# Kernel tuning notes

Hardware: AMD Instinct MI355X
Metric: run time of the kernel (lower is better)

## Reference

```python
import jax, jax.numpy as jnp
import numpy as np

D = 256        # embedding_dim
K = 4096       # num_embeddings
DECAY = 0.99
EPS = 1e-05
COMMIT = 0.25


def setup_inputs() -> dict:
    key = jax.random.key(0)
    kx, ke = jax.random.split(key)
    x = jax.random.normal(kx, (32, 1024, D), dtype=jnp.float32)
    # variance_scaling(scale=1.0, mode='fan_in', distribution='uniform') on (D, K): fan_in = D
    limit = np.sqrt(3.0 / D).astype(np.float32)
    embeddings = jax.random.uniform(ke, (D, K), dtype=jnp.float32, minval=-limit, maxval=limit)
    return {
        'x': x,
        'embeddings': embeddings,
        'ema_counter': jnp.zeros((), jnp.float32),
        'ema_hidden_cluster': jnp.zeros((K,), jnp.float32),
        'ema_hidden_dw': jnp.zeros((D, K), jnp.float32),
    }


def reference(x, embeddings, ema_counter, ema_hidden_cluster, ema_hidden_dw):
    flat = x.reshape(-1, D)  # [N, D]
    # squared euclidean distance to each code: [N, K]
    distance = (jnp.sum(flat ** 2, axis=1, keepdims=True)
                - 2.0 * jnp.matmul(flat, embeddings)
                + jnp.sum(embeddings ** 2, axis=0, keepdims=True))
    encoding_indices = jnp.argmax(-distance, axis=1)           # [N]
    encodings = jax.nn.one_hot(encoding_indices, K, dtype=distance.dtype)  # [N, K]
    idx = encoding_indices.reshape(x.shape[:-1])               # [B, T]
    quantized = jnp.take(embeddings.T, idx, axis=0)            # [B, T, D]

    e_latent_loss = jnp.mean((quantized - x) ** 2)
    q_latent_loss = jnp.mean((quantized - x) ** 2)
    vq_loss = q_latent_loss + COMMIT * e_latent_loss

    # EMA codebook update (training=True path); debiased EMA per the module
    counter = ema_counter + 1.0
    bias = 1.0 - jnp.power(DECAY, counter)
    cluster_hidden = ema_hidden_cluster * DECAY + jnp.sum(encodings, axis=0) * (1.0 - DECAY)
    cluster_avg = cluster_hidden / bias                         # [K]
    dw = jnp.matmul(flat.T, encodings)                          # [D, K]
    dw_hidden = ema_hidden_dw * DECAY + dw * (1.0 - DECAY)
    dw_avg = dw_hidden / bias                                   # [D, K]
    n = jnp.sum(cluster_avg)
    cluster_norm = (cluster_avg + EPS) / (n + K * EPS) * n
    new_embeddings = dw_avg / cluster_norm[None, :]             # [D, K]

    avg_probs = jnp.mean(encodings, axis=0)
    perplexity = jnp.exp(-jnp.sum(avg_probs * jnp.log(avg_probs + 1e-10)))
    return quantized, vq_loss, perplexity, idx, new_embeddings
```

## Files before the change

### kernel.cpp

```cpp
#include <hip/hip_runtime.h>
#include <math.h>

#define N_TOK 32768
#define DIM   256
#define KCODE 4096

#define WS_E2      0
#define WS_COUNTS  4096
#define WS_LOSSP   8192
#define WS_SCAL    8448
#define WS_CNORM   8512
#define WS_IDX     12608
#define WS_EHS     307520
#define WS_DWT     1356096
#define WS_CARRYV  2404672
#define WS_CARRYI  2437440
#define WS_OFFS    2470208
#define WS_WOFF    2474304

#define OUT_Q      0
#define OUT_LOSS   8388608
#define OUT_PERP   8388609
#define OUT_IDX    8388610
#define OUT_EMB    8421378

#define EH_PLANE   1048576

typedef _Float16 f16x8 __attribute__((ext_vector_type(8)));
typedef _Float16 f16x4 __attribute__((ext_vector_type(4)));
typedef float    f32x4 __attribute__((ext_vector_type(4)));

__global__ void k_split_e(const float* __restrict__ emb, unsigned short* __restrict__ ehs_,
                          float* __restrict__ e2)
{
    __shared__ float tile[32][33];
    _Float16* ehs = (_Float16*)ehs_;
    int t  = threadIdx.x;
    int tx = t & 31, iy = t >> 5;
    int k0 = blockIdx.x * 32, d0 = blockIdx.y * 32;
#pragma unroll
    for (int j = 0; j < 4; ++j)
        tile[iy + 8 * j][tx] = emb[(size_t)(d0 + iy + 8 * j) * KCODE + k0 + tx];
    __syncthreads();
    int code = k0 + tx;
    size_t base = (size_t)(((code >> 8) * 8) + (d0 >> 5)) * 8192 + (code & 255) * 32 + iy * 4;
    f16x4 h1, h2;
    float ssq = 0.0f;
#pragma unroll
    for (int j = 0; j < 4; ++j) {
        float v = tile[iy * 4 + j][tx];
        ssq += v * v;
        _Float16 a = (_Float16)v;
        h1[j] = a;
        h2[j] = (_Float16)(v - (float)a);
    }
    *(f16x4*)(ehs + base)            = h1;
    *(f16x4*)(ehs + EH_PLANE + base) = h2;
    atomicAdd(&e2[code], ssq);
}

__global__ __launch_bounds__(256, 2)
void k_argmin(const float* __restrict__ x, const unsigned short* __restrict__ ehs_,
              const float* __restrict__ e2, int* __restrict__ idx_out,
              float* __restrict__ carryV, int* __restrict__ carryI,
              float* __restrict__ out_idxf, float* __restrict__ counts,
              int ct0, int phase)
{
    __shared__ __align__(16) _Float16 Ah[2][64][256];

    const _Float16* ehs = (const _Float16*)ehs_;

    const int t    = threadIdx.x;
    const int lane = t & 63, w = t >> 6;
    const int lo   = lane & 15, q = lane >> 4;
    const int row0 = blockIdx.x * 64;

    {
        int m = t >> 3, kb = (t & 7) * 32;
#pragma unroll
        for (int rr = 0; rr < 2; ++rr) {
            int mm = m + 32 * rr;
            const float* src = x + (size_t)(row0 + mm) * DIM + kb;
#pragma unroll
            for (int g = 0; g < 4; ++g) {
                f32x4 f0 = __builtin_nontemporal_load((const f32x4*)(src + g * 8));
                f32x4 f1 = __builtin_nontemporal_load((const f32x4*)(src + g * 8 + 4));
                f16x8 h1, h2;
#pragma unroll
                for (int j = 0; j < 4; ++j) {
                    _Float16 a = (_Float16)f0[j];
                    h1[j] = a; h2[j] = (_Float16)(f0[j] - (float)a);
                    _Float16 b = (_Float16)f1[j];
                    h1[j + 4] = b; h2[j + 4] = (_Float16)(f1[j] - (float)b);
                }
                int grp = ((kb >> 3) + g) ^ (mm & 7);
                *(f16x8*)&Ah[0][mm][grp * 8] = h1;
                *(f16x8*)&Ah[1][mm][grp * 8] = h2;
            }
        }
    }
    __syncthreads();

    float best[16];
    int   bidx[16];
#pragma unroll
    for (int s = 0; s < 16; ++s) { best[s] = 3.4e38f; bidx[s] = 0; }

    const _Float16* ehp1 = ehs + (size_t)(w * 64 + lo) * 32 + q * 8;
    const _Float16* ehp2 = ehp1 + EH_PLANE;

    f16x8 b1f[2][4], b2f[2][4];

    {
        const size_t so0 = (size_t)(ct0 * 8) * 8192;
#pragma unroll
        for (int nf = 0; nf < 4; ++nf) {
            b1f[0][nf] = *(const f16x8*)(ehp1 + so0 + nf * 512);
            b2f[0][nf] = *(const f16x8*)(ehp2 + so0 + nf * 512);
        }
    }

    for (int ct = ct0; ct < ct0 + 8; ++ct) {
        float e2r[4];
#pragma unroll
        for (int nf = 0; nf < 4; ++nf)
            e2r[nf] = e2[ct * 256 + w * 64 + nf * 16 + lo];

        f32x4 acc[4][4];
#pragma unroll
        for (int mf = 0; mf < 4; ++mf)
#pragma unroll
            for (int nf = 0; nf < 4; ++nf) acc[mf][nf] = (f32x4)0.0f;

#pragma unroll
        for (int ks = 0; ks < 8; ++ks) {
            const int cur = ks & 1, nxt = cur ^ 1;
            const int so  = ct * 8 + ks;

            if (ks < 7 || ct < ct0 + 7) {
                const size_t po = (size_t)(so + 1) * 8192;
#pragma unroll
                for (int nf = 0; nf < 4; ++nf) {
                    b1f[nxt][nf] = *(const f16x8*)(ehp1 + po + nf * 512);
                    b2f[nxt][nf] = *(const f16x8*)(ehp2 + po + nf * 512);
                }
            }
            __builtin_amdgcn_sched_barrier(0);

            const int agrp = ((ks * 4 + q) ^ (lo & 7)) * 8;
            f16x8 a1[4], a2[4];
#pragma unroll
            for (int mf = 0; mf < 4; ++mf)
                a2[mf] = *(const f16x8*)&Ah[1][mf * 16 + lo][agrp];
#pragma unroll
            for (int mf = 0; mf < 4; ++mf)
                a1[mf] = *(const f16x8*)&Ah[0][mf * 16 + lo][agrp];

#pragma unroll
            for (int nf = 0; nf < 4; ++nf) {
#pragma unroll
                for (int mf = 0; mf < 4; ++mf)
                    acc[mf][nf] = __builtin_amdgcn_mfma_f32_16x16x32_f16(a2[mf], b1f[cur][nf], acc[mf][nf], 0, 0, 0);
#pragma unroll
                for (int mf = 0; mf < 4; ++mf)
                    acc[mf][nf] = __builtin_amdgcn_mfma_f32_16x16x32_f16(a1[mf], b2f[cur][nf], acc[mf][nf], 0, 0, 0);
#pragma unroll
                for (int mf = 0; mf < 4; ++mf)
                    acc[mf][nf] = __builtin_amdgcn_mfma_f32_16x16x32_f16(a1[mf], b1f[cur][nf], acc[mf][nf], 0, 0, 0);
            }
        }

#pragma unroll
        for (int nf = 0; nf < 4; ++nf) {
            int cl = w * 64 + nf * 16 + lo;
            float e2v = e2r[nf];
#pragma unroll
            for (int mf = 0; mf < 4; ++mf)
#pragma unroll
                for (int r = 0; r < 4; ++r) {
                    float dist = fmaf(-2.0f, acc[mf][nf][r], e2v);
                    int s = mf * 4 + r;
                    if (dist < best[s]) { best[s] = dist; bidx[s] = ct * 256 + cl; }
                }
        }
    }

    __syncthreads();
    float* rv = (float*)&Ah[0][0][0];
    int*   ri = (int*)(((char*)&Ah[0][0][0]) + 16384);
#pragma unroll
    for (int s = 0; s < 16; ++s) {
        int row = (s >> 2) * 16 + q * 4 + (s & 3);
        rv[row * 64 + w * 16 + lo] = best[s];
        ri[row * 64 + w * 16 + lo] = bidx[s];
    }
    __syncthreads();
    if (t < 64) {
        float bv; int bi;
        if (phase) { bv = carryV[row0 + t]; bi = carryI[row0 + t]; }
        else       { bv = 3.4e38f; bi = 0x40000000; }
        for (int jj = 0; jj < 64; ++jj) {
            int j = (jj + t) & 63;
            float v = rv[t * 64 + j];
            int  ii = ri[t * 64 + j];
            if (v < bv || (v == bv && ii < bi)) { bv = v; bi = ii; }
        }
        if (phase) {
            idx_out[row0 + t] = bi;
            out_idxf[row0 + t] = (float)bi;
            atomicAdd(&counts[bi], 1.0f);
        } else {
            carryV[row0 + t] = bv; carryI[row0 + t] = bi;
        }
    }
}

__global__ void k_scan(const float* __restrict__ counts, int* __restrict__ offs,
                       int* __restrict__ woff)
{
    __shared__ int ps[256];
    int t = threadIdx.x;
    int local[16];
    int s = 0;
#pragma unroll
    for (int j = 0; j < 16; ++j) {
        local[j] = s;
        s += (int)counts[t * 16 + j];
    }
    ps[t] = s;
    __syncthreads();
    for (int off = 1; off < 256; off <<= 1) {
        int v = (t >= off) ? ps[t - off] : 0;
        __syncthreads();
        ps[t] += v;
        __syncthreads();
    }
    int base = (t > 0) ? ps[t - 1] : 0;
#pragma unroll
    for (int j = 0; j < 16; ++j) {
        int o = base + local[j];
        offs[t * 16 + j] = o;
        woff[t * 16 + j] = o;
    }
}

__global__ void k_scatter(const int* __restrict__ idx, int* __restrict__ woff,
                          int* __restrict__ rowlist)
{
    int n = blockIdx.x * 256 + threadIdx.x;
    int k = idx[n];
    int pos = atomicAdd(&woff[k], 1);
    rowlist[pos] = n;
}

__global__ void k_dw(const float* __restrict__ x, const unsigned short* __restrict__ ehs_,
                     const int* __restrict__ rowlist, const int* __restrict__ offs,
                     const float* __restrict__ counts, float* __restrict__ dwT,
                     float* __restrict__ out_q, float* __restrict__ lossp)
{
    __shared__ __align__(16) float es[256];
    __shared__ __align__(16) float red[4][256];
    const _Float16* ehs = (const _Float16*)ehs_;
    int k = blockIdx.x, t = threadIdx.x;
    int lane = t & 63, w = t >> 6;
    size_t base = (size_t)(((k >> 8) * 8) + (t >> 5)) * 8192 + (k & 255) * 32 + (t & 31);
    float e = (float)ehs[base] + (float)ehs[EH_PLANE + base];
    es[t] = e;
    int start = offs[k];
    int cnt   = (int)counts[k];
    __syncthreads();
    float4 ev = *(const float4*)&es[lane * 4];
    float4 acc = {0.0f, 0.0f, 0.0f, 0.0f};
    float sq = 0.0f;
    for (int j = w; j < cnt; j += 4) {
        int n = rowlist[start + j];
        float4 xv = *(const float4*)&x[(size_t)n * DIM + lane * 4];
        acc.x += xv.x; acc.y += xv.y; acc.z += xv.z; acc.w += xv.w;
        sq += xv.x * xv.x + xv.y * xv.y + xv.z * xv.z + xv.w * xv.w;
        *(float4*)&out_q[(size_t)n * DIM + lane * 4] = ev;
    }
    *(float4*)&red[w][lane * 4] = acc;
    __syncthreads();
    float s = red[0][t] + red[1][t] + red[2][t] + red[3][t];
    dwT[(size_t)k * DIM + t] = s;
    float v1 = es[t] * s;
    float v2 = e * e;
    float v3 = sq;
#pragma unroll
    for (int off = 32; off > 0; off >>= 1) {
        v1 += __shfl_down(v1, off, 64);
        v2 += __shfl_down(v2, off, 64);
        v3 += __shfl_down(v3, off, 64);
    }
    __syncthreads();
    if (lane == 0) { red[0][w] = v1; red[1][w] = v2; red[2][w] = v3; }
    __syncthreads();
    if (t == 0 && cnt > 0) {
        float dot = red[0][0] + red[0][1] + red[0][2] + red[0][3];
        float e2t = red[1][0] + red[1][1] + red[1][2] + red[1][3];
        float sqt = red[2][0] + red[2][1] + red[2][2] + red[2][3];
        atomicAdd(&lossp[k & 255], (float)cnt * e2t - 2.0f * dot + sqt);
    }
}

__global__ void k_finalize(const float* __restrict__ counts, const float* __restrict__ lossp,
                           const float* __restrict__ ema_counter,
                           const float* __restrict__ ema_cluster,
                           float* __restrict__ cnorm, float* __restrict__ scal,
                           float* __restrict__ out)
{
    __shared__ float red[256];
    int t = threadIdx.x;
    float ls = lossp[t];
    float ent = 0.0f, casum = 0.0f;
    float ca[16];
#pragma unroll
    for (int j = 0; j < 16; ++j) {
        int k = j * 256 + t;
        float c = counts[k];
        float p = c * (1.0f / 32768.0f);
        ent += p * logf(p + 1e-10f);
        ca[j] = ema_cluster[k] * 0.99f + c * 0.01f;
        casum += ca[j];
    }
    red[t] = ls; __syncthreads();
    for (int o = 128; o > 0; o >>= 1) { if (t < o) red[t] += red[t + o]; __syncthreads(); }
    float loss_tot = red[0]; __syncthreads();
    red[t] = ent; __syncthreads();
    for (int o = 128; o > 0; o >>= 1) { if (t < o) red[t] += red[t + o]; __syncthreads(); }
    float ent_tot = red[0]; __syncthreads();
    red[t] = casum; __syncthreads();
    for (int o = 128; o > 0; o >>= 1) { if (t < o) red[t] += red[t + o]; __syncthreads(); }
    float casum_tot = red[0]; __syncthreads();

    float bias = 1.0f - powf(0.99f, ema_counter[0] + 1.0f);
    float n = casum_tot / bias;
    float inv = n / (n + 4096.0f * 1e-5f);
#pragma unroll
    for (int j = 0; j < 16; ++j) {
        int k = j * 256 + t;
        cnorm[k] = (ca[j] / bias + 1e-5f) * inv;
    }
    if (t == 0) {
        out[OUT_LOSS] = 1.25f * loss_tot * (1.0f / (32768.0f * 256.0f));
        out[OUT_PERP] = expf(-ent_tot);
        scal[0] = bias;
    }
}

__global__ void k_newemb(const float* __restrict__ dwT, const float* __restrict__ ema_dw,
                         const float* __restrict__ cnorm, const float* __restrict__ scal,
                         float* __restrict__ out_emb)
{
    __shared__ float tile[32][33];
    int t = threadIdx.x;
    int tx = t & 31, iy = t >> 5;
    int k0 = blockIdx.x * 32, d0 = blockIdx.y * 32;
#pragma unroll
    for (int j = 0; j < 4; ++j)
        tile[iy + 8 * j][tx] = dwT[(size_t)(k0 + iy + 8 * j) * DIM + d0 + tx];
    __syncthreads();
    float inv_bias = 1.0f / scal[0];
    float cn = cnorm[k0 + tx];
#pragma unroll
    for (int j = 0; j < 4; ++j) {
        int d = d0 + iy + 8 * j;
        float dwv = tile[tx][iy + 8 * j];
        float hid = ema_dw[(size_t)d * KCODE + k0 + tx] * 0.99f + dwv * 0.01f;
        out_emb[(size_t)d * KCODE + k0 + tx] = hid * inv_bias / cn;
    }
}

extern "C" void kernel_launch(void* const* d_in, const int* in_sizes, int n_in,
                              void* d_out, int out_size, void* d_ws, size_t ws_size,
                              hipStream_t stream)
{
    const float* x           = (const float*)d_in[0];
    const float* emb         = (const float*)d_in[1];
    const float* ema_counter = (const float*)d_in[2];
    const float* ema_cluster = (const float*)d_in[3];
    const float* ema_dw      = (const float*)d_in[4];
    float* out = (float*)d_out;
    float* ws  = (float*)d_ws;

    float* e2     = ws + WS_E2;
    float* counts = ws + WS_COUNTS;
    float* lossp  = ws + WS_LOSSP;
    float* scal   = ws + WS_SCAL;
    float* cnorm  = ws + WS_CNORM;
    int*   idxw   = (int*)(ws + WS_IDX);
    unsigned short* ehs = (unsigned short*)(ws + WS_EHS);
    float* dwT    = ws + WS_DWT;
    float* carryV = ws + WS_CARRYV;
    int*   carryI = (int*)(ws + WS_CARRYI);
    int*   rowlist= (int*)(ws + WS_CARRYV);
    int*   offs   = (int*)(ws + WS_OFFS);
    int*   woff   = (int*)(ws + WS_WOFF);

    hipMemsetAsync(e2, 0, (size_t)WS_CNORM * sizeof(float), stream);

    k_split_e<<<dim3(128, 8), 256, 0, stream>>>(emb, ehs, e2);
    k_argmin<<<512, 256, 0, stream>>>(x, ehs, e2, idxw, carryV, carryI,
                                      out + OUT_IDX, counts, 0, 0);
    k_argmin<<<512, 256, 0, stream>>>(x, ehs, e2, idxw, carryV, carryI,
                                      out + OUT_IDX, counts, 8, 1);
    k_scan<<<1, 256, 0, stream>>>(counts, offs, woff);
    k_scatter<<<128, 256, 0, stream>>>(idxw, woff, rowlist);
    k_dw<<<4096, 256, 0, stream>>>(x, ehs, rowlist, offs, counts, dwT,
                                   out + OUT_Q, lossp);
    k_finalize<<<1, 256, 0, stream>>>(counts, lossp, ema_counter, ema_cluster,
                                      cnorm, scal, out);
    k_newemb<<<dim3(128, 8), 256, 0, stream>>>(dwT, ema_dw, cnorm, scal, out + OUT_EMB);
}
```

Measured before the change: 316.2 us.

## Double argmin block to 512 threads with narrower per-wave code tiles

Raises the argmin kernel from 4 to 8 waves per block, with each wave covering 32 codes per tile instead of 64. This halves the accumulator and B-fragment registers per wave. The software double-buffered prefetch of the codebook fragments is dropped in favour of more waves hiding latency. The final reduction now scans 128 partial results per row, and the x staging loop drops from two rows per thread to one. The risks are losing the explicit prefetch overlap and a longer serial reduction.

```diff
diff --git a/kernel.cpp b/kernel.cpp
--- a/kernel.cpp
+++ b/kernel.cpp
@@ -59,7 +59,7 @@
     atomicAdd(&e2[code], ssq);
 }
 
-__global__ __launch_bounds__(256, 2)
+__global__ __launch_bounds__(512, 2)
 void k_argmin(const float* __restrict__ x, const unsigned short* __restrict__ ehs_,
               const float* __restrict__ e2, int* __restrict__ idx_out,
               float* __restrict__ carryV, int* __restrict__ carryI,
@@ -77,26 +77,22 @@
 
     {
         int m = t >> 3, kb = (t & 7) * 32;
-#pragma unroll
-        for (int rr = 0; rr < 2; ++rr) {
-            int mm = m + 32 * rr;
-            const float* src = x + (size_t)(row0 + mm) * DIM + kb;
-#pragma unroll
-            for (int g = 0; g < 4; ++g) {
-                f32x4 f0 = __builtin_nontemporal_load((const f32x4*)(src + g * 8));
-                f32x4 f1 = __builtin_nontemporal_load((const f32x4*)(src + g * 8 + 4));
-                f16x8 h1, h2;
-#pragma unroll
-                for (int j = 0; j < 4; ++j) {
-                    _Float16 a = (_Float16)f0[j];
-                    h1[j] = a; h2[j] = (_Float16)(f0[j] - (float)a);
-                    _Float16 b = (_Float16)f1[j];
-                    h1[j + 4] = b; h2[j + 4] = (_Float16)(f1[j] - (float)b);
-                }
-                int grp = ((kb >> 3) + g) ^ (mm & 7);
-                *(f16x8*)&Ah[0][mm][grp * 8] = h1;
-                *(f16x8*)&Ah[1][mm][grp * 8] = h2;
+        const float* src = x + (size_t)(row0 + m) * DIM + kb;
+#pragma unroll
+        for (int g = 0; g < 4; ++g) {
+            f32x4 f0 = __builtin_nontemporal_load((const f32x4*)(src + g * 8));
+            f32x4 f1 = __builtin_nontemporal_load((const f32x4*)(src + g * 8 + 4));
+            f16x8 h1, h2;
+#pragma unroll
+            for (int j = 0; j < 4; ++j) {
+                _Float16 a = (_Float16)f0[j];
+                h1[j] = a; h2[j] = (_Float16)(f0[j] - (float)a);
+                _Float16 b = (_Float16)f1[j];
+                h1[j + 4] = b; h2[j + 4] = (_Float16)(f1[j] - (float)b);
             }
+            int grp = ((kb >> 3) + g) ^ (m & 7);
+            *(f16x8*)&Ah[0][m][grp * 8] = h1;
+            *(f16x8*)&Ah[1][m][grp * 8] = h2;
         }
     }
     __syncthreads();
@@ -106,73 +102,57 @@
 #pragma unroll
     for (int s = 0; s < 16; ++s) { best[s] = 3.4e38f; bidx[s] = 0; }
 
-    const _Float16* ehp1 = ehs + (size_t)(w * 64 + lo) * 32 + q * 8;
+    const _Float16* ehp1 = ehs + (size_t)(w * 32 + lo) * 32 + q * 8;
     const _Float16* ehp2 = ehp1 + EH_PLANE;
 
-    f16x8 b1f[2][4], b2f[2][4];
-
-    {
-        const size_t so0 = (size_t)(ct0 * 8) * 8192;
-#pragma unroll
-        for (int nf = 0; nf < 4; ++nf) {
-            b1f[0][nf] = *(const f16x8*)(ehp1 + so0 + nf * 512);
-            b2f[0][nf] = *(const f16x8*)(ehp2 + so0 + nf * 512);
-        }
-    }
-
     for (int ct = ct0; ct < ct0 + 8; ++ct) {
-        float e2r[4];
-#pragma unroll
-        for (int nf = 0; nf < 4; ++nf)
-            e2r[nf] = e2[ct * 256 + w * 64 + nf * 16 + lo];
-
-        f32x4 acc[4][4];
+        float e2r[2];
+#pragma unroll
+        for (int nf = 0; nf < 2; ++nf)
+            e2r[nf] = e2[ct * 256 + w * 32 + nf * 16 + lo];
+
+        f32x4 acc[4][2];
 #pragma unroll
         for (int mf = 0; mf < 4; ++mf)
 #pragma unroll
-            for (int nf = 0; nf < 4; ++nf) acc[mf][nf] = (f32x4)0.0f;
+            for (int nf = 0; nf < 2; ++nf) acc[mf][nf] = (f32x4)0.0f;
 
 #pragma unroll
         for (int ks = 0; ks < 8; ++ks) {
-            const int cur = ks & 1, nxt = cur ^ 1;
-            const int so  = ct * 8 + ks;
-
-            if (ks < 7 || ct < ct0 + 7) {
-                const size_t po = (size_t)(so + 1) * 8192;
-#pragma unroll
-                for (int nf = 0; nf < 4; ++nf) {
-                    b1f[nxt][nf] = *(const f16x8*)(ehp1 + po + nf * 512);
-                    b2f[nxt][nf] = *(const f16x8*)(ehp2 + po + nf * 512);
-                }
+            const size_t so = (size_t)(ct * 8 + ks) * 8192;
+
+            f16x8 b1[2], b2[2];
+#pragma unroll
+            for (int nf = 0; nf < 2; ++nf) {
+                b1[nf] = *(const f16x8*)(ehp1 + so + nf * 512);
+                b2[nf] = *(const f16x8*)(ehp2 + so + nf * 512);
             }
-            __builtin_amdgcn_sched_barrier(0);
 
             const int agrp = ((ks * 4 + q) ^ (lo & 7)) * 8;
             f16x8 a1[4], a2[4];
 #pragma unroll
-            for (int mf = 0; mf < 4; ++mf)
+            for (int mf = 0; mf < 4; ++mf) {
                 a2[mf] = *(const f16x8*)&Ah[1][mf * 16 + lo][agrp];
-#pragma unroll
-            for (int mf = 0; mf < 4; ++mf)
                 a1[mf] = *(const f16x8*)&Ah[0][mf * 16 + lo][agrp];
-
-#pragma unroll
-            for (int nf = 0; nf < 4; ++nf) {
+            }
+
+#pragma unroll
+            for (int nf = 0; nf < 2; ++nf) {
 #pragma unroll
                 for (int mf = 0; mf < 4; ++mf)
-                    acc[mf][nf] = __builtin_amdgcn_mfma_f32_16x16x32_f16(a2[mf], b1f[cur][nf], acc[mf][nf], 0, 0, 0);
+                    acc[mf][nf] = __builtin_amdgcn_mfma_f32_16x16x32_f16(a2[mf], b1[nf], acc[mf][nf], 0, 0, 0);
 #pragma unroll
                 for (int mf = 0; mf < 4; ++mf)
-                    acc[mf][nf] = __builtin_amdgcn_mfma_f32_16x16x32_f16(a1[mf], b2f[cur][nf], acc[mf][nf], 0, 0, 0);
+                    acc[mf][nf] = __builtin_amdgcn_mfma_f32_16x16x32_f16(a1[mf], b2[nf], acc[mf][nf], 0, 0, 0);
 #pragma unroll
                 for (int mf = 0; mf < 4; ++mf)
-                    acc[mf][nf] = __builtin_amdgcn_mfma_f32_16x16x32_f16(a1[mf], b1f[cur][nf], acc[mf][nf], 0, 0, 0);
+                    acc[mf][nf] = __builtin_amdgcn_mfma_f32_16x16x32_f16(a1[mf], b1[nf], acc[mf][nf], 0, 0, 0);
             }
         }
 
 #pragma unroll
-        for (int nf = 0; nf < 4; ++nf) {
-            int cl = w * 64 + nf * 16 + lo;
+        for (int nf = 0; nf < 2; ++nf) {
+            int cl = w * 32 + nf * 16 + lo;
             float e2v = e2r[nf];
 #pragma unroll
             for (int mf = 0; mf < 4; ++mf)
@@ -187,22 +167,22 @@
 
     __syncthreads();
     float* rv = (float*)&Ah[0][0][0];
-    int*   ri = (int*)(((char*)&Ah[0][0][0]) + 16384);
+    int*   ri = (int*)(((char*)&Ah[0][0][0]) + 32768);
 #pragma unroll
     for (int s = 0; s < 16; ++s) {
         int row = (s >> 2) * 16 + q * 4 + (s & 3);
-        rv[row * 64 + w * 16 + lo] = best[s];
-        ri[row * 64 + w * 16 + lo] = bidx[s];
+        rv[row * 128 + w * 16 + lo] = best[s];
+        ri[row * 128 + w * 16 + lo] = bidx[s];
     }
     __syncthreads();
     if (t < 64) {
         float bv; int bi;
         if (phase) { bv = carryV[row0 + t]; bi = carryI[row0 + t]; }
         else       { bv = 3.4e38f; bi = 0x40000000; }
-        for (int jj = 0; jj < 64; ++jj) {
-            int j = (jj + t) & 63;
-            float v = rv[t * 64 + j];
-            int  ii = ri[t * 64 + j];
+        for (int jj = 0; jj < 128; ++jj) {
+            int j = (jj + t * 2) & 127;
+            float v = rv[t * 128 + j];
+            int  ii = ri[t * 128 + j];
             if (v < bv || (v == bv && ii < bi)) { bv = v; bi = ii; }
         }
         if (phase) {
@@ -400,9 +380,9 @@
     hipMemsetAsync(e2, 0, (size_t)WS_CNORM * sizeof(float), stream);
 
     k_split_e<<<dim3(128, 8), 256, 0, stream>>>(emb, ehs, e2);
-    k_argmin<<<512, 256, 0, stream>>>(x, ehs, e2, idxw, carryV, carryI,
+    k_argmin<<<512, 512, 0, stream>>>(x, ehs, e2, idxw, carryV, carryI,
                                       out + OUT_IDX, counts, 0, 0);
-    k_argmin<<<512, 256, 0, stream>>>(x, ehs, e2, idxw, carryV, carryI,
+    k_argmin<<<512, 512, 0, stream>>>(x, ehs, e2, idxw, carryV, carryI,
                                       out + OUT_IDX, counts, 8, 1);
     k_scan<<<1, 256, 0, stream>>>(counts, offs, woff);
     k_scatter<<<128, 256, 0, stream>>>(idxw, woff, rowlist);
```

After: 605.7 us. 1.92x slower.

## Fuse quantized output and loss into argmin; merge scan with finalize

Applied to the files above, without the earlier changes.

The second argmin pass now computes the per-row squared norm of x while staging it, derives each row's loss as best distance plus that norm, and writes the quantized rows directly from the split-fp16 codebook. The scan and finalize kernels are merged into a single one-block kernel. k_dw is reduced to the dw accumulation only. This removes the scattered out_q writes and the per-code loss work from k_dw and saves one launch, at the cost of a longer argmin epilogue and a loss computed from the fp16-split distance. The tie-break on equal distances is also made to prefer the lower index.

```diff
diff --git a/kernel.cpp b/kernel.cpp
--- a/kernel.cpp
+++ b/kernel.cpp
@@ -64,9 +64,12 @@
               const float* __restrict__ e2, int* __restrict__ idx_out,
               float* __restrict__ carryV, int* __restrict__ carryI,
               float* __restrict__ out_idxf, float* __restrict__ counts,
+              float* __restrict__ lossp, float* __restrict__ out_q,
               int ct0, int phase)
 {
     __shared__ __align__(16) _Float16 Ah[2][64][256];
+    __shared__ float xsqp[64][8];
+    __shared__ int   bis[64];
 
     const _Float16* ehs = (const _Float16*)ehs_;
 
@@ -77,10 +80,12 @@
 
     {
         int m = t >> 3, kb = (t & 7) * 32;
+        float ssq0 = 0.0f, ssq1 = 0.0f;
 #pragma unroll
         for (int rr = 0; rr < 2; ++rr) {
             int mm = m + 32 * rr;
             const float* src = x + (size_t)(row0 + mm) * DIM + kb;
+            float ss = 0.0f;
 #pragma unroll
             for (int g = 0; g < 4; ++g) {
                 f32x4 f0 = __builtin_nontemporal_load((const f32x4*)(src + g * 8));
@@ -88,6 +93,7 @@
                 f16x8 h1, h2;
 #pragma unroll
                 for (int j = 0; j < 4; ++j) {
+                    ss += f0[j] * f0[j] + f1[j] * f1[j];
                     _Float16 a = (_Float16)f0[j];
                     h1[j] = a; h2[j] = (_Float16)(f0[j] - (float)a);
                     _Float16 b = (_Float16)f1[j];
@@ -97,14 +103,17 @@
                 *(f16x8*)&Ah[0][mm][grp * 8] = h1;
                 *(f16x8*)&Ah[1][mm][grp * 8] = h2;
             }
-        }
+            if (rr == 0) ssq0 = ss; else ssq1 = ss;
+        }
+        xsqp[m][t & 7]      = ssq0;
+        xsqp[m + 32][t & 7] = ssq1;
     }
     __syncthreads();
 
     float best[16];
     int   bidx[16];
 #pragma unroll
-    for (int s = 0; s < 16; ++s) { best[s] = 3.4e38f; bidx[s] = 0; }
+    for (int s = 0; s < 16; ++s) { best[s] = 3.4e38f; bidx[s] = 0x40000000; }
 
     const _Float16* ehp1 = ehs + (size_t)(w * 64 + lo) * 32 + q * 8;
     const _Float16* ehp2 = ehp1 + EH_PLANE;
@@ -172,7 +181,7 @@
 
 #pragma unroll
         for (int nf = 0; nf < 4; ++nf) {
-            int cl = w * 64 + nf * 16 + lo;
+            int ci = ct * 256 + w * 64 + nf * 16 + lo;
             float e2v = e2r[nf];
 #pragma unroll
             for (int mf = 0; mf < 4; ++mf)
@@ -180,7 +189,9 @@
                 for (int r = 0; r < 4; ++r) {
                     float dist = fmaf(-2.0f, acc[mf][nf][r], e2v);
                     int s = mf * 4 + r;
-                    if (dist < best[s]) { best[s] = dist; bidx[s] = ct * 256 + cl; }
+                    if (dist < best[s] || (dist == best[s] && ci < bidx[s])) {
+                        best[s] = dist; bidx[s] = ci;
+                    }
                 }
         }
     }
@@ -209,17 +220,59 @@
             idx_out[row0 + t] = bi;
             out_idxf[row0 + t] = (float)bi;
             atomicAdd(&counts[bi], 1.0f);
+            bis[t] = bi;
+            float xsq = 0.0f;
+#pragma unroll
+            for (int j = 0; j < 8; ++j) xsq += xsqp[t][j];
+            float lr = bv + xsq;
+#pragma unroll
+            for (int off = 32; off > 0; off >>= 1) lr += __shfl_down(lr, off, 64);
+            if (t == 0) atomicAdd(&lossp[blockIdx.x & 255], lr);
         } else {
             carryV[row0 + t] = bv; carryI[row0 + t] = bi;
         }
     }
-}
-
-__global__ void k_scan(const float* __restrict__ counts, int* __restrict__ offs,
-                       int* __restrict__ woff)
-{
-    __shared__ int ps[256];
+    if (phase) {
+        __syncthreads();
+        int r  = t >> 2, qs = t & 3;
+        int k  = bis[r];
+        float* dst = out_q + (size_t)(row0 + r) * DIM + qs * 64;
+        const _Float16* ehb = ehs + (size_t)((k >> 8) * 8 + qs * 2) * 8192 + (k & 255) * 32;
+#pragma unroll
+        for (int dd = 0; dd < 2; ++dd) {
+            const _Float16* p1 = ehb + dd * 8192;
+            const _Float16* p2 = p1 + EH_PLANE;
+#pragma unroll
+            for (int g = 0; g < 4; ++g) {
+                f16x8 h1 = *(const f16x8*)(p1 + g * 8);
+                f16x8 h2 = *(const f16x8*)(p2 + g * 8);
+                float4 o0, o1;
+                o0.x = (float)h1[0] + (float)h2[0];
+                o0.y = (float)h1[1] + (float)h2[1];
+                o0.z = (float)h1[2] + (float)h2[2];
+                o0.w = (float)h1[3] + (float)h2[3];
+                o1.x = (float)h1[4] + (float)h2[4];
+                o1.y = (float)h1[5] + (float)h2[5];
+                o1.z = (float)h1[6] + (float)h2[6];
+                o1.w = (float)h1[7] + (float)h2[7];
+                *(float4*)(dst + dd * 32 + g * 8)     = o0;
+                *(float4*)(dst + dd * 32 + g * 8 + 4) = o1;
+            }
+        }
+    }
+}
+
+__global__ void k_scanfin(const float* __restrict__ counts, const float* __restrict__ lossp,
+                          const float* __restrict__ ema_counter,
+                          const float* __restrict__ ema_cluster,
+                          int* __restrict__ offs, int* __restrict__ woff,
+                          float* __restrict__ cnorm, float* __restrict__ scal,
+                          float* __restrict__ out)
+{
+    __shared__ int   ps[256];
+    __shared__ float red[256];
     int t = threadIdx.x;
+
     int local[16];
     int s = 0;
 #pragma unroll
@@ -242,75 +295,7 @@
         offs[t * 16 + j] = o;
         woff[t * 16 + j] = o;
     }
-}
-
-__global__ void k_scatter(const int* __restrict__ idx, int* __restrict__ woff,
-                          int* __restrict__ rowlist)
-{
-    int n = blockIdx.x * 256 + threadIdx.x;
-    int k = idx[n];
-    int pos = atomicAdd(&woff[k], 1);
-    rowlist[pos] = n;
-}
-
-__global__ void k_dw(const float* __restrict__ x, const unsigned short* __restrict__ ehs_,
-                     const int* __restrict__ rowlist, const int* __restrict__ offs,
-                     const float* __restrict__ counts, float* __restrict__ dwT,
-                     float* __restrict__ out_q, float* __restrict__ lossp)
-{
-    __shared__ __align__(16) float es[256];
-    __shared__ __align__(16) float red[4][256];
-    const _Float16* ehs = (const _Float16*)ehs_;
-    int k = blockIdx.x, t = threadIdx.x;
-    int lane = t & 63, w = t >> 6;
-    size_t base = (size_t)(((k >> 8) * 8) + (t >> 5)) * 8192 + (k & 255) * 32 + (t & 31);
-    float e = (float)ehs[base] + (float)ehs[EH_PLANE + base];
-    es[t] = e;
-    int start = offs[k];
-    int cnt   = (int)counts[k];
-    __syncthreads();
-    float4 ev = *(const float4*)&es[lane * 4];
-    float4 acc = {0.0f, 0.0f, 0.0f, 0.0f};
-    float sq = 0.0f;
-    for (int j = w; j < cnt; j += 4) {
-        int n = rowlist[start + j];
-        float4 xv = *(const float4*)&x[(size_t)n * DIM + lane * 4];
-        acc.x += xv.x; acc.y += xv.y; acc.z += xv.z; acc.w += xv.w;
-        sq += xv.x * xv.x + xv.y * xv.y + xv.z * xv.z + xv.w * xv.w;
-        *(float4*)&out_q[(size_t)n * DIM + lane * 4] = ev;
-    }
-    *(float4*)&red[w][lane * 4] = acc;
-    __syncthreads();
-    float s = red[0][t] + red[1][t] + red[2][t] + red[3][t];
-    dwT[(size_t)k * DIM + t] = s;
-    float v1 = es[t] * s;
-    float v2 = e * e;
-    float v3 = sq;
-#pragma unroll
-    for (int off = 32; off > 0; off >>= 1) {
-        v1 += __shfl_down(v1, off, 64);
-        v2 += __shfl_down(v2, off, 64);
-        v3 += __shfl_down(v3, off, 64);
-    }
-    __syncthreads();
-    if (lane == 0) { red[0][w] = v1; red[1][w] = v2; red[2][w] = v3; }
-    __syncthreads();
-    if (t == 0 && cnt > 0) {
-        float dot = red[0][0] + red[0][1] + red[0][2] + red[0][3];
-        float e2t = red[1][0] + red[1][1] + red[1][2] + red[1][3];
-        float sqt = red[2][0] + red[2][1] + red[2][2] + red[2][3];
-        atomicAdd(&lossp[k & 255], (float)cnt * e2t - 2.0f * dot + sqt);
-    }
-}
-
-__global__ void k_finalize(const float* __restrict__ counts, const float* __restrict__ lossp,
-                           const float* __restrict__ ema_counter,
-                           const float* __restrict__ ema_cluster,
-                           float* __restrict__ cnorm, float* __restrict__ scal,
-                           float* __restrict__ out)
-{
-    __shared__ float red[256];
-    int t = threadIdx.x;
+
     float ls = lossp[t];
     float ent = 0.0f, casum = 0.0f;
     float ca[16];
@@ -323,6 +308,7 @@
         ca[j] = ema_cluster[k] * 0.99f + c * 0.01f;
         casum += ca[j];
     }
+    __syncthreads();
     red[t] = ls; __syncthreads();
     for (int o = 128; o > 0; o >>= 1) { if (t < o) red[t] += red[t + o]; __syncthreads(); }
     float loss_tot = red[0]; __syncthreads();
@@ -346,6 +332,36 @@
         out[OUT_PERP] = expf(-ent_tot);
         scal[0] = bias;
     }
+}
+
+__global__ void k_scatter(const int* __restrict__ idx, int* __restrict__ woff,
+                          int* __restrict__ rowlist)
+{
+    int n = blockIdx.x * 256 + threadIdx.x;
+    int k = idx[n];
+    int pos = atomicAdd(&woff[k], 1);
+    rowlist[pos] = n;
+}
+
+__global__ void k_dw(const float* __restrict__ x, const int* __restrict__ rowlist,
+                     const int* __restrict__ offs, const float* __restrict__ counts,
+                     float* __restrict__ dwT)
+{
+    __shared__ __align__(16) float red[4][256];
+    int k = blockIdx.x, t = threadIdx.x;
+    int lane = t & 63, w = t >> 6;
+    int start = offs[k];
+    int cnt   = (int)counts[k];
+    float4 acc = {0.0f, 0.0f, 0.0f, 0.0f};
+    for (int j = w; j < cnt; j += 4) {
+        int n = rowlist[start + j];
+        float4 xv = *(const float4*)&x[(size_t)n * DIM + lane * 4];
+        acc.x += xv.x; acc.y += xv.y; acc.z += xv.z; acc.w += xv.w;
+    }
+    *(float4*)&red[w][lane * 4] = acc;
+    __syncthreads();
+    float s = red[0][t] + red[1][t] + red[2][t] + red[3][t];
+    dwT[(size_t)k * DIM + t] = s;
 }
 
 __global__ void k_newemb(const float* __restrict__ dwT, const float* __restrict__ ema_dw,
@@ -401,14 +417,12 @@
 
     k_split_e<<<dim3(128, 8), 256, 0, stream>>>(emb, ehs, e2);
     k_argmin<<<512, 256, 0, stream>>>(x, ehs, e2, idxw, carryV, carryI,
-                                      out + OUT_IDX, counts, 0, 0);
+                                      out + OUT_IDX, counts, lossp, out + OUT_Q, 0, 0);
     k_argmin<<<512, 256, 0, stream>>>(x, ehs, e2, idxw, carryV, carryI,
-                                      out + OUT_IDX, counts, 8, 1);
-    k_scan<<<1, 256, 0, stream>>>(counts, offs, woff);
+                                      out + OUT_IDX, counts, lossp, out + OUT_Q, 8, 1);
+    k_scanfin<<<1, 256, 0, stream>>>(counts, lossp, ema_counter, ema_cluster,
+                                     offs, woff, cnorm, scal, out);
     k_scatter<<<128, 256, 0, stream>>>(idxw, woff, rowlist);
-    k_dw<<<4096, 256, 0, stream>>>(x, ehs, rowlist, offs, counts, dwT,
-                                   out + OUT_Q, lossp);
-    k_finalize<<<1, 256, 0, stream>>>(counts, lossp, ema_counter, ema_cluster,
-                                      cnorm, scal, out);
+    k_dw<<<4096, 256, 0, stream>>>(x, rowlist, offs, counts, dwT);
     k_newemb<<<dim3(128, 8), 256, 0, stream>>>(dwT, ema_dw, cnorm, scal, out + OUT_EMB);
 }
```

Measured after the change: 334.4 us. 1.06x slower.
